# Performance work log

Measured on AMD Instinct MI355X. Metric: run time of the kernel, lower is better.

Reference implementation:

```python
import jax, jax.numpy as jnp
import numpy as np

N_NODES = 100000


def _gcn_conv(x, edge_index, W, b, n_nodes):
    # PyG GCNConv: add self-loops, symmetric normalization, linear, aggregate, bias.
    src, dst = edge_index[0], edge_index[1]
    loop = jnp.arange(n_nodes, dtype=src.dtype)
    src = jnp.concatenate([src, loop])
    dst = jnp.concatenate([dst, loop])
    deg = jax.ops.segment_sum(jnp.ones_like(dst, dtype=x.dtype), dst, num_segments=n_nodes)
    dinv = jax.lax.rsqrt(jnp.maximum(deg, 1.0))  # deg >= 1 due to self-loops
    norm = dinv[src] * dinv[dst]                 # [E+N]
    h = x @ W                                    # [N, out]
    msg = h[src] * norm[:, None]                 # [E+N, out] gather
    out = jax.ops.segment_sum(msg, dst, num_segments=n_nodes)  # scatter-add
    return out + b


def setup_inputs() -> dict:
    key = jax.random.key(0)
    k1, k2, k3, k4, k5 = jax.random.split(key, 5)
    in_c, hid = 128, 64
    x = jax.random.normal(k1, (N_NODES, in_c), dtype=jnp.float32)
    edge_index = jax.random.randint(k2, (2, 1600000), 0, N_NODES, dtype=jnp.int64)
    s1 = 1.0 / np.sqrt(in_c)
    s2 = 1.0 / np.sqrt(2 * hid)
    W1 = jax.random.uniform(k3, (in_c, 2 * hid), jnp.float32, -s1, s1)
    b1 = jnp.zeros((2 * hid,), jnp.float32)
    W2 = jax.random.uniform(k4, (2 * hid, hid), jnp.float32, -s2, s2)
    b2 = jnp.zeros((hid,), jnp.float32)
    return {"x": x, "edge_index": edge_index, "W1": W1, "b1": b1, "W2": W2, "b2": b2}


def reference(x, edge_index, W1, b1, W2, b2):
    h = jax.nn.relu(_gcn_conv(x, edge_index, W1, b1, N_NODES))
    return _gcn_conv(h, edge_index, W2, b2, N_NODES)
```

## Files before the change

### kernel.cpp

```cpp
#include <hip/hip_runtime.h>
#include <hip/hip_fp16.h>
#include <cstdint>

constexpr int K_IN = 128;
constexpr int N_H1 = 128;
constexpr int N_H2 = 64;

constexpr int NPR      = 128;
constexpr int NREG_PAD = 800;
constexpr int BCHUNKS  = 128;

__device__ __forceinline__ void store_h4(__half* p, float4 v) {
    __half2 a = __floats2half2_rn(v.x, v.y), b = __floats2half2_rn(v.z, v.w);
    uint2 u;
    u.x = *(unsigned*)&a; u.y = *(unsigned*)&b;
    *(uint2*)p = u;
}
__device__ __forceinline__ void acc_h8(float* acc, uint4 u) {
    const __half2* h = (const __half2*)&u;
    #pragma unroll
    for (int i = 0; i < 4; ++i) {
        float2 f = __half22float2(h[i]);
        acc[2 * i]     += f.x;
        acc[2 * i + 1] += f.y;
    }
}
__device__ __forceinline__ void init_h8(float* acc, uint4 u) {
    const __half2* h = (const __half2*)&u;
    #pragma unroll
    for (int i = 0; i < 4; ++i) {
        float2 f = __half22float2(h[i]);
        acc[2 * i]     = f.x;
        acc[2 * i + 1] = f.y;
    }
}


__launch_bounds__(256)
__global__ void hist_kernel(const int* __restrict__ dst, int* __restrict__ hist,
                            int E, int nreg, int chunk) {
    __shared__ int h[NREG_PAD];
    const int tid = threadIdx.x, b = blockIdx.x;
    for (int i = tid; i < nreg; i += 256) h[i] = 0;
    __syncthreads();
    const int lo = b * chunk, hi = min(lo + chunk, E);
    for (int i = lo + tid; i < hi; i += 256) atomicAdd(&h[dst[i] >> 7], 1);
    __syncthreads();
    for (int i = tid; i < nreg; i += 256) hist[(long)b * nreg + i] = h[i];
}


__launch_bounds__(BCHUNKS)
__global__ void rscan_kernel(int* __restrict__ hist, int* __restrict__ totals, int nreg) {
    __shared__ int sh[BCHUNKS];
    const int r = blockIdx.x, t = threadIdx.x;
    int v = hist[(long)t * nreg + r];
    sh[t] = v;
    __syncthreads();
    #pragma unroll
    for (int off = 1; off < BCHUNKS; off <<= 1) {
        int u = (t >= off) ? sh[t - off] : 0;
        __syncthreads();
        sh[t] += u;
        __syncthreads();
    }
    hist[(long)t * nreg + r] = sh[t] - v;
    if (t == BCHUNKS - 1) totals[r] = sh[t];
}


__launch_bounds__(1024)
__global__ void tscan_kernel(const int* __restrict__ totals, int* __restrict__ wbase, int nreg) {
    __shared__ int sh[1024];
    const int t = threadIdx.x;
    int v = (t < nreg) ? totals[t] : 0;
    sh[t] = v;
    __syncthreads();
    #pragma unroll
    for (int off = 1; off < 1024; off <<= 1) {
        int u = (t >= off) ? sh[t - off] : 0;
        __syncthreads();
        sh[t] += u;
        __syncthreads();
    }
    if (t < nreg) wbase[t] = sh[t] - v;
}


__launch_bounds__(256)
__global__ void scatter_kernel(const int* __restrict__ src, const int* __restrict__ dst,
                               const int* __restrict__ hist, const int* __restrict__ wbase,
                               int* __restrict__ pedge, int E, int nreg, int chunk) {
    __shared__ int cur[NREG_PAD];
    __shared__ int wb[NREG_PAD];
    const int tid = threadIdx.x, b = blockIdx.x;
    for (int i = tid; i < nreg; i += 256) {
        cur[i] = hist[(long)b * nreg + i];
        wb[i]  = wbase[i];
    }
    __syncthreads();
    const int lo = b * chunk, hi = min(lo + chunk, E);
    for (int i = lo + tid; i < hi; i += 256) {
        int d = dst[i];
        int r = d >> 7;
        int p = atomicAdd(&cur[r], 1);
        pedge[wb[r] + p] = ((d & (NPR - 1)) << 17) | src[i];
    }
}


__launch_bounds__(256)
__global__ void csr_build_kernel(const int* __restrict__ totals, const int* __restrict__ wbase,
                                 const int* __restrict__ pedge,
                                 int* __restrict__ pos, int* __restrict__ cnt,
                                 float* __restrict__ dinv, int* __restrict__ ssrc, int n) {
    __shared__ int cnt_l[NPR];
    __shared__ int scan_l[NPR];
    __shared__ int pos_mut[NPR];

    const int r   = blockIdx.x;
    const int tid = threadIdx.x;
    const int wb  = wbase[r];
    const int ne  = totals[r];

    if (tid < NPR) cnt_l[tid] = 0;
    __syncthreads();

    const int* pe = &pedge[wb];
    for (int j = tid; j < ne; j += 256) atomicAdd(&cnt_l[pe[j] >> 17], 1);
    __syncthreads();

    if (tid < NPR) scan_l[tid] = cnt_l[tid];
    __syncthreads();
    #pragma unroll
    for (int off = 1; off < NPR; off <<= 1) {
        int v = (tid < NPR && tid >= off) ? scan_l[tid - off] : 0;
        __syncthreads();
        if (tid < NPR) scan_l[tid] += v;
        __syncthreads();
    }
    if (tid < NPR) {
        int excl = scan_l[tid] - cnt_l[tid];
        pos_mut[tid] = excl;
        int node = r * NPR + tid;
        if (node < n) {
            pos[node]  = wb + excl;
            cnt[node]  = cnt_l[tid];
            dinv[node] = rsqrtf((float)cnt_l[tid] + 1.0f);
        }
    }
    __syncthreads();

    int* so = &ssrc[wb];
    for (int j = tid; j < ne; j += 256) {
        int v  = pe[j];
        int p  = atomicAdd(&pos_mut[v >> 17], 1);
        so[p]  = v & 0x1FFFF;
    }
}


__launch_bounds__(256)
__global__ void gemm1_kernel(const float* __restrict__ X, const float* __restrict__ W,
                             const float* __restrict__ dinv,
                             __half* __restrict__ H, int nrows) {
    constexpr int K     = 128;
    constexpr int NOUT  = 128;
    constexpr int TN    = 8;
    constexpr int NJ    = 2;
    constexpr int TM    = 4;
    constexpr int BROWS = 64;
    constexpr int PASSES = BROWS * K / 4 / 256;

    __shared__ float Ws[K * NOUT];
    __shared__ float xs[BROWS * K];

    const int tid = threadIdx.x;
    const int rt  = tid / 16;
    const int ct  = tid % 16;

    for (int i = tid * 4; i < K * NOUT; i += 256 * 4)
        *(float4*)&Ws[i] = *(const float4*)&W[i];

    for (long row0 = (long)blockIdx.x * BROWS; row0 < nrows;
         row0 += (long)gridDim.x * BROWS) {
        __syncthreads();

        #pragma unroll
        for (int p = 0; p < PASSES; ++p) {
            int flat = tid + p * 256;
            int row  = flat >> 5;
            int c4   = flat & 31;
            long grow = row0 + row;
            if (grow >= nrows) grow = nrows - 1;
            float4 v = *(const float4*)&X[grow * K + c4 * 4];
            int koff = (c4 * 4) ^ ((row & 7) << 2);
            *(float4*)&xs[row * K + koff] = v;
        }
        __syncthreads();

        float acc[TM][TN];
        #pragma unroll
        for (int m = 0; m < TM; ++m)
            #pragma unroll
            for (int n = 0; n < TN; ++n) acc[m][n] = 0.f;

        #pragma unroll 2
        for (int k0 = 0; k0 < K; k0 += 4) {
            float4 xv[TM];
            #pragma unroll
            for (int m = 0; m < TM; ++m) {
                int r = rt + 16 * m;
                xv[m] = *(const float4*)&xs[r * K + (k0 ^ ((r & 7) << 2))];
            }
            float4 wv[4][NJ];
            #pragma unroll
            for (int kk = 0; kk < 4; ++kk)
                #pragma unroll
                for (int j = 0; j < NJ; ++j)
                    wv[kk][j] = *(const float4*)&Ws[(k0 + kk) * NOUT + ct * 4 + j * 64];

            #pragma unroll
            for (int m = 0; m < TM; ++m) {
                float xk[4] = {xv[m].x, xv[m].y, xv[m].z, xv[m].w};
                #pragma unroll
                for (int kk = 0; kk < 4; ++kk) {
                    #pragma unroll
                    for (int j = 0; j < NJ; ++j) {
                        acc[m][4*j+0] += xk[kk] * wv[kk][j].x;
                        acc[m][4*j+1] += xk[kk] * wv[kk][j].y;
                        acc[m][4*j+2] += xk[kk] * wv[kk][j].z;
                        acc[m][4*j+3] += xk[kk] * wv[kk][j].w;
                    }
                }
            }
        }

        #pragma unroll
        for (int m = 0; m < TM; ++m) {
            long grow = row0 + rt + 16 * m;
            if (grow < nrows) {
                float sc = dinv[grow];
                #pragma unroll
                for (int j = 0; j < NJ; ++j) {
                    float4 o = { acc[m][4*j+0] * sc, acc[m][4*j+1] * sc,
                                 acc[m][4*j+2] * sc, acc[m][4*j+3] * sc };
                    store_h4(&H[grow * NOUT + ct * 4 + j * 64], o);
                }
            }
        }
    }
}


__launch_bounds__(256)
__global__ void fused_l2_kernel(const int* __restrict__ pos, const int* __restrict__ cnt,
                                const int* __restrict__ ssrc,
                                const float* __restrict__ dinv, const __half* __restrict__ h1h,
                                const float* __restrict__ b1, const float* __restrict__ W2,
                                __half* __restrict__ h2h, int n) {
    __shared__ float qs[16][132];

    const int tid  = threadIdx.x;
    const int g    = tid >> 4;
    const int sub  = tid & 15;
    const int base = blockIdx.x * 16;

    {
        int node = base + g;
        if (node < n) {
            int deg = cnt[node];
            const int* bu = &ssrc[pos[node]];
            float acc[8];
            init_h8(acc, *(const uint4*)&h1h[(long)node * 128 + sub * 8]);
            int j = 0;
            for (; j + 3 < deg; j += 4) {
                int s0 = bu[j], s1 = bu[j + 1], s2 = bu[j + 2], s3 = bu[j + 3];
                uint4 v0 = *(const uint4*)&h1h[(long)s0 * 128 + sub * 8];
                uint4 v1 = *(const uint4*)&h1h[(long)s1 * 128 + sub * 8];
                uint4 v2 = *(const uint4*)&h1h[(long)s2 * 128 + sub * 8];
                uint4 v3 = *(const uint4*)&h1h[(long)s3 * 128 + sub * 8];
                acc_h8(acc, v0); acc_h8(acc, v1); acc_h8(acc, v2); acc_h8(acc, v3);
            }
            for (; j < deg; ++j) {
                uint4 v = *(const uint4*)&h1h[(long)bu[j] * 128 + sub * 8];
                acc_h8(acc, v);
            }
            float dv  = dinv[node];
            float4 ba = *(const float4*)&b1[sub * 8];
            float4 bb = *(const float4*)&b1[sub * 8 + 4];
            float4 q0, q1;
            q0.x = fmaxf(dv * (dv * acc[0] + ba.x), 0.f);
            q0.y = fmaxf(dv * (dv * acc[1] + ba.y), 0.f);
            q0.z = fmaxf(dv * (dv * acc[2] + ba.z), 0.f);
            q0.w = fmaxf(dv * (dv * acc[3] + ba.w), 0.f);
            q1.x = fmaxf(dv * (dv * acc[4] + bb.x), 0.f);
            q1.y = fmaxf(dv * (dv * acc[5] + bb.y), 0.f);
            q1.z = fmaxf(dv * (dv * acc[6] + bb.z), 0.f);
            q1.w = fmaxf(dv * (dv * acc[7] + bb.w), 0.f);
            *(float4*)&qs[g][sub * 8]     = q0;
            *(float4*)&qs[g][sub * 8 + 4] = q1;
        }
    }
    __syncthreads();

    {
        const int bn = tid >> 4;
        const int c4 = tid & 15;
        int node = base + bn;
        if (node < n) {
            float4 acc = {0.f, 0.f, 0.f, 0.f};
            #pragma unroll 4
            for (int k0 = 0; k0 < 128; k0 += 4) {
                float4 q4 = *(const float4*)&qs[bn][k0];
                float qk[4] = {q4.x, q4.y, q4.z, q4.w};
                #pragma unroll
                for (int kk = 0; kk < 4; ++kk) {
                    float4 w = *(const float4*)&W2[(k0 + kk) * 64 + c4 * 4];
                    acc.x += qk[kk] * w.x; acc.y += qk[kk] * w.y;
                    acc.z += qk[kk] * w.z; acc.w += qk[kk] * w.w;
                }
            }
            store_h4(&h2h[(long)node * 64 + c4 * 4], acc);
        }
    }
}


__launch_bounds__(256)
__global__ void agg2_kernel(const int* __restrict__ pos, const int* __restrict__ cnt,
                            const int* __restrict__ ssrc,
                            const float* __restrict__ dinv, const __half* __restrict__ Hs,
                            const float* __restrict__ bias, float* __restrict__ OUT, int n) {
    const int tid  = threadIdx.x;
    const int node = blockIdx.x * 32 + (tid >> 3);
    const int sub  = tid & 7;
    if (node >= n) return;

    int deg = cnt[node];
    const int* bu = &ssrc[pos[node]];

    float acc[8];
    init_h8(acc, *(const uint4*)&Hs[(long)node * 64 + sub * 8]);
    int j = 0;
    for (; j + 3 < deg; j += 4) {
        int s0 = bu[j], s1 = bu[j + 1], s2 = bu[j + 2], s3 = bu[j + 3];
        uint4 v0 = *(const uint4*)&Hs[(long)s0 * 64 + sub * 8];
        uint4 v1 = *(const uint4*)&Hs[(long)s1 * 64 + sub * 8];
        uint4 v2 = *(const uint4*)&Hs[(long)s2 * 64 + sub * 8];
        uint4 v3 = *(const uint4*)&Hs[(long)s3 * 64 + sub * 8];
        acc_h8(acc, v0); acc_h8(acc, v1); acc_h8(acc, v2); acc_h8(acc, v3);
    }
    for (; j < deg; ++j) {
        uint4 v = *(const uint4*)&Hs[(long)bu[j] * 64 + sub * 8];
        acc_h8(acc, v);
    }

    const float d = dinv[node];
    float4 ba = *(const float4*)&bias[sub * 8];
    float4 bb = *(const float4*)&bias[sub * 8 + 4];
    float4 o0 = { acc[0] * d + ba.x, acc[1] * d + ba.y,
                  acc[2] * d + ba.z, acc[3] * d + ba.w };
    float4 o1 = { acc[4] * d + bb.x, acc[5] * d + bb.y,
                  acc[6] * d + bb.z, acc[7] * d + bb.w };
    *(float4*)&OUT[(long)node * 64 + sub * 8]     = o0;
    *(float4*)&OUT[(long)node * 64 + sub * 8 + 4] = o1;
}


extern "C" void kernel_launch(void* const* d_in, const int* in_sizes, int n_in,
                              void* d_out, int out_size, void* d_ws, size_t ws_size,
                              hipStream_t stream) {
    const float* x   = (const float*)d_in[0];
    const int*   ei  = (const int*)d_in[1];
    const float* W1  = (const float*)d_in[2];
    const float* b1  = (const float*)d_in[3];
    const float* W2  = (const float*)d_in[4];
    const float* b2  = (const float*)d_in[5];
    float*       out = (float*)d_out;

    const int N = in_sizes[0] / K_IN;
    const int E = in_sizes[1] / 2;

    const int* esrc = ei;
    const int* edst = ei + E;

    const int NREG  = (N + NPR - 1) / NPR;
    const int CHUNK = (E + BCHUNKS - 1) / BCHUNKS;

    char*   ws     = (char*)d_ws;
    int*    hist   = (int*)ws;
    int*    totals = hist + (size_t)BCHUNKS * NREG;
    int*    wbase  = totals + NREG_PAD;
    int*    pos    = wbase + NREG_PAD;
    int*    cnt    = pos + N;
    float*  dinv   = (float*)(cnt + N);
    int*    pedge  = (int*)(dinv + N);
    int*    ssrc   = pedge + E;
    __half* h1h    = (__half*)(ssrc + E);
    __half* h2h    = h1h + (size_t)N * N_H1;

    hist_kernel<<<BCHUNKS, 256, 0, stream>>>(edst, hist, E, NREG, CHUNK);
    rscan_kernel<<<NREG, BCHUNKS, 0, stream>>>(hist, totals, NREG);
    tscan_kernel<<<1, 1024, 0, stream>>>(totals, wbase, NREG);
    scatter_kernel<<<BCHUNKS, 256, 0, stream>>>(esrc, edst, hist, wbase, pedge, E, NREG, CHUNK);
    csr_build_kernel<<<NREG, 256, 0, stream>>>(totals, wbase, pedge, pos, cnt, dinv, ssrc, N);

    gemm1_kernel<<<256, 256, 0, stream>>>(x, W1, dinv, h1h, N);

    fused_l2_kernel<<<(N + 15) / 16, 256, 0, stream>>>(pos, cnt, ssrc, dinv, h1h, b1, W2, h2h, N);

    agg2_kernel<<<(N + 31) / 32, 256, 0, stream>>>(pos, cnt, ssrc, dinv, h2h, b2, out, N);
}
```

Baseline: 288.9 us.

## Sort nodes by degree within regions to balance aggregation warps

During CSR construction each 128-node region bitonic-sorts its nodes by in-degree and writes a permutation array. The layer-2 fused and final aggregation kernels then process nodes in this order, so nodes of similar degree share a wavefront and divergence from uneven loop trip counts drops. The edge-scatter chunk count is also doubled. In exchange the sort adds barriers to csr_build, the permutation adds an indirect load, and output writes become less contiguous. With random uniform edges the degree spread is modest, which limits what the reordering can gain.

New measurement: 289.8 us. Within noise of the previous version (+0.3%).

```diff
diff --git a/kernel.cpp b/kernel.cpp
--- a/kernel.cpp
+++ b/kernel.cpp
@@ -8,7 +8,7 @@
 
 constexpr int NPR      = 128;
 constexpr int NREG_PAD = 800;
-constexpr int BCHUNKS  = 128;
+constexpr int BCHUNKS  = 256;
 
 __device__ __forceinline__ void store_h4(__half* p, float4 v) {
     __half2 a = __floats2half2_rn(v.x, v.y), b = __floats2half2_rn(v.z, v.w);
@@ -113,10 +113,12 @@
 __global__ void csr_build_kernel(const int* __restrict__ totals, const int* __restrict__ wbase,
                                  const int* __restrict__ pedge,
                                  int* __restrict__ pos, int* __restrict__ cnt,
-                                 float* __restrict__ dinv, int* __restrict__ ssrc, int n) {
+                                 float* __restrict__ dinv, int* __restrict__ ssrc,
+                                 int* __restrict__ order, int n) {
     __shared__ int cnt_l[NPR];
     __shared__ int scan_l[NPR];
     __shared__ int pos_mut[NPR];
+    __shared__ int key_l[NPR];
 
     const int r   = blockIdx.x;
     const int tid = threadIdx.x;
@@ -148,14 +150,31 @@
             cnt[node]  = cnt_l[tid];
             dinv[node] = rsqrtf((float)cnt_l[tid] + 1.0f);
         }
-    }
+        key_l[tid] = (((node < n) ? cnt_l[tid] : 0x7FFF) << 7) | tid;
+    }
+    __syncthreads();
+
+    for (int k = 2; k <= NPR; k <<= 1) {
+        for (int j = k >> 1; j > 0; j >>= 1) {
+            if (tid < NPR) {
+                int ixj = tid ^ j;
+                if (ixj > tid) {
+                    int a = key_l[tid], b = key_l[ixj];
+                    bool asc = ((tid & k) == 0);
+                    if (asc ? (a > b) : (a < b)) { key_l[tid] = b; key_l[ixj] = a; }
+                }
+            }
+            __syncthreads();
+        }
+    }
+    if (tid < NPR) order[r * NPR + tid] = r * NPR + (key_l[tid] & 127);
     __syncthreads();
 
     int* so = &ssrc[wb];
     for (int j = tid; j < ne; j += 256) {
-        int v  = pe[j];
-        int p  = atomicAdd(&pos_mut[v >> 17], 1);
-        so[p]  = v & 0x1FFFF;
+        int v = pe[j];
+        int p = atomicAdd(&pos_mut[v >> 17], 1);
+        so[p] = v & 0x1FFFF;
     }
 }
 
@@ -254,20 +273,25 @@
 
 
 __launch_bounds__(256)
-__global__ void fused_l2_kernel(const int* __restrict__ pos, const int* __restrict__ cnt,
+__global__ void fused_l2_kernel(const int* __restrict__ order,
+                                const int* __restrict__ pos, const int* __restrict__ cnt,
                                 const int* __restrict__ ssrc,
                                 const float* __restrict__ dinv, const __half* __restrict__ h1h,
                                 const float* __restrict__ b1, const float* __restrict__ W2,
                                 __half* __restrict__ h2h, int n) {
     __shared__ float qs[16][132];
+    __shared__ int   node_l[16];
 
     const int tid  = threadIdx.x;
     const int g    = tid >> 4;
     const int sub  = tid & 15;
     const int base = blockIdx.x * 16;
 
+    if (tid < 16) node_l[tid] = order[base + tid];
+    __syncthreads();
+
     {
-        int node = base + g;
+        int node = node_l[g];
         if (node < n) {
             int deg = cnt[node];
             const int* bu = &ssrc[pos[node]];
@@ -307,7 +331,7 @@
     {
         const int bn = tid >> 4;
         const int c4 = tid & 15;
-        int node = base + bn;
+        int node = node_l[bn];
         if (node < n) {
             float4 acc = {0.f, 0.f, 0.f, 0.f};
             #pragma unroll 4
@@ -328,12 +352,13 @@
 
 
 __launch_bounds__(256)
-__global__ void agg2_kernel(const int* __restrict__ pos, const int* __restrict__ cnt,
+__global__ void agg2_kernel(const int* __restrict__ order,
+                            const int* __restrict__ pos, const int* __restrict__ cnt,
                             const int* __restrict__ ssrc,
                             const float* __restrict__ dinv, const __half* __restrict__ Hs,
                             const float* __restrict__ bias, float* __restrict__ OUT, int n) {
     const int tid  = threadIdx.x;
-    const int node = blockIdx.x * 32 + (tid >> 3);
+    const int node = order[blockIdx.x * 32 + (tid >> 3)];
     const int sub  = tid & 7;
     if (node >= n) return;
 
@@ -395,7 +420,8 @@
     int*    pos    = wbase + NREG_PAD;
     int*    cnt    = pos + N;
     float*  dinv   = (float*)(cnt + N);
-    int*    pedge  = (int*)(dinv + N);
+    int*    order  = (int*)(dinv + N);
+    int*    pedge  = order + (size_t)NREG * NPR;
     int*    ssrc   = pedge + E;
     __half* h1h    = (__half*)(ssrc + E);
     __half* h2h    = h1h + (size_t)N * N_H1;
@@ -404,11 +430,11 @@
     rscan_kernel<<<NREG, BCHUNKS, 0, stream>>>(hist, totals, NREG);
     tscan_kernel<<<1, 1024, 0, stream>>>(totals, wbase, NREG);
     scatter_kernel<<<BCHUNKS, 256, 0, stream>>>(esrc, edst, hist, wbase, pedge, E, NREG, CHUNK);
-    csr_build_kernel<<<NREG, 256, 0, stream>>>(totals, wbase, pedge, pos, cnt, dinv, ssrc, N);
+    csr_build_kernel<<<NREG, 256, 0, stream>>>(totals, wbase, pedge, pos, cnt, dinv, ssrc, order, N);
 
     gemm1_kernel<<<256, 256, 0, stream>>>(x, W1, dinv, h1h, N);
 
-    fused_l2_kernel<<<(N + 15) / 16, 256, 0, stream>>>(pos, cnt, ssrc, dinv, h1h, b1, W2, h2h, N);
-
-    agg2_kernel<<<(N + 31) / 32, 256, 0, stream>>>(pos, cnt, ssrc, dinv, h2h, b2, out, N);
-}
+    fused_l2_kernel<<<(N + 15) / 16, 256, 0, stream>>>(order, pos, cnt, ssrc, dinv, h1h, b1, W2, h2h, N);
+
+    agg2_kernel<<<(N + 31) / 32, 256, 0, stream>>>(order, pos, cnt, ssrc, dinv, h2h, b2, out, N);
+}
```
